# Performance work log

Measured on AMD Instinct MI355X. Metric: run time of the kernel, lower is better.

Reference implementation:

```python
import jax, jax.numpy as jnp
import numpy as np

TOKEN_ATTEND_SELF_VALUE = -0.0005
LN_EPS = 1e-5


def _layer_norm(x, g, b):
    mu = jnp.mean(x, axis=-1, keepdims=True)
    var = jnp.mean(jnp.square(x - mu), axis=-1, keepdims=True)
    return (x - mu) * jax.lax.rsqrt(var + LN_EPS) * g + b


def _gelu(x):
    return jax.nn.gelu(x, approximate=False)  # torch nn.GELU default is exact erf


def _grouped_ff(x, w1, b1, w2, b2):
    # x: [b, n, L, d]; per-level (grouped conv1d k=1) feedforward
    h = _gelu(jnp.einsum('bnld,ldm->bnlm', x, w1) + b1)
    return _gelu(jnp.einsum('bnlm,lmd->bnld', h, w2) + b2)


def _consensus_attention(levels):
    # levels: [b, n, L, d]; attend_self=False, no local mask
    b, n, L, d = levels.shape
    norm = jnp.maximum(jnp.linalg.norm(levels, axis=-1, keepdims=True), 1e-12)
    k = levels / norm  # F.normalize(dim=-1)
    sim = jnp.einsum('bild,bjld->blij', levels, k) * (d ** -0.5)
    eye = jnp.eye(n, dtype=bool)[None, None, :, :]
    sim = jnp.where(eye, TOKEN_ATTEND_SELF_VALUE, sim)
    attn = jax.nn.softmax(sim, axis=-1)
    return jnp.einsum('blij,bjld->bild', attn, levels)


def setup_inputs() -> dict:
    key = jax.random.key(0)
    ks = jax.random.split(key, 12)
    B, C, H, W = 2, 3, 48, 48
    dim, L = 32, 5
    n = H * W  # sub_patch_size = 1
    s = 0.02
    inp = {
        'img': jax.random.normal(ks[0], (B, C, H, W), jnp.float32),
        'w_tok': jax.random.normal(ks[1], (C, dim), jnp.float32) * s,
        'b_tok': jnp.zeros((dim,), jnp.float32),
        'g_ln_tok': jnp.ones((dim,), jnp.float32),
        'b_ln_tok': jnp.zeros((dim,), jnp.float32),
        'w_lvl': jax.random.normal(ks[2], (C, L * dim), jnp.float32) * s,
        'b_lvl': jnp.zeros((L * dim,), jnp.float32),
        'g_ln_lvl': jnp.ones((dim,), jnp.float32),
        'b_ln_lvl': jnp.zeros((dim,), jnp.float32),
        'pos_emb': jax.random.normal(ks[3], (n, dim), jnp.float32) * s,
        'bu_w1': jax.random.normal(ks[4], (L, dim, 4 * dim), jnp.float32) * s,
        'bu_b1': jnp.zeros((L, 4 * dim), jnp.float32),
        'bu_w2': jax.random.normal(ks[5], (L, 4 * dim, dim), jnp.float32) * s,
        'bu_b2': jnp.zeros((L, dim), jnp.float32),
        'td_w1': jax.random.normal(ks[6], (L - 1, dim, 4 * dim), jnp.float32) * s,
        'td_b1': jnp.zeros((L - 1, 4 * dim), jnp.float32),
        'td_w2': jax.random.normal(ks[7], (L - 1, 4 * dim, dim), jnp.float32) * s,
        'td_b2': jnp.zeros((L - 1, dim), jnp.float32),
        'iters': 3,
    }
    return inp


def reference(img, w_tok, b_tok, g_ln_tok, b_ln_tok, w_lvl, b_lvl, g_ln_lvl,
              b_ln_lvl, pos_emb, bu_w1, bu_b1, bu_w2, bu_b2, td_w1, td_b1,
              td_w2, td_b2, iters):
    B, C, H, W = img.shape
    L = bu_w1.shape[0]
    dim = w_tok.shape[1]
    x = jnp.transpose(img, (0, 2, 3, 1)).reshape(B, H * W, C)  # b n c

    # image_to_tokens: Linear -> LayerNorm -> GELU
    tokens = _gelu(_layer_norm(x @ w_tok + b_tok, g_ln_tok, b_ln_tok))  # [b,n,d]

    # image_to_levels: 1x1 Conv -> GELU -> reshape -> LayerNorm
    lv = _gelu(x @ w_lvl + b_lvl).reshape(B, H * W, L, dim)
    levels = _layer_norm(lv, g_ln_lvl, b_ln_lvl)  # [b,n,L,d]

    pos = pos_emb[None, :, None, :]  # () n () d
    bottom = tokens[:, :, None, :]  # [b,n,1,d]

    num_contrib = jnp.array([4.0] * (L - 1) + [3.0], jnp.float32)[None, None, :, None]

    for _ in range(iters):
        lwi = jnp.concatenate([bottom, levels], axis=2)  # [b,n,L+1,d]
        bu = _grouped_ff(lwi[:, :, :-1, :], bu_w1, bu_b1, bu_w2, bu_b2)
        td = _grouped_ff(lwi[:, :, 2:, :] + pos, td_w1, td_b1, td_w2, td_b2)
        td = jnp.pad(td, ((0, 0), (0, 0), (0, 1), (0, 0)))  # zero at top level
        cons = _consensus_attention(levels)
        levels = (levels + bu + td + cons) / num_contrib

    return levels
```

## Files before the change

### kernel.cpp

```cpp
#include <hip/hip_runtime.h>
#include <math.h>

#define BB 2
#define NN 2304
#define DIM 32
#define LL 5
#define HID 128
#define SJ 6
#define BLN (BB * LL * NN)
#define CONSGRID (SJ * 18 * LL * BB)
#define FFGRID (9 * 36)

#define QK_SCALE2 0.25503486f
#define SELF_VAL2 (-7.2134752e-4f)

typedef __attribute__((ext_vector_type(8))) short bf16x8;
typedef __attribute__((ext_vector_type(16))) float f32x16;

union B8U { bf16x8 v; unsigned u[4]; };

__device__ __forceinline__ unsigned bfb(float f) {
    union { float f; unsigned u; } c; c.f = f;
    return ((c.u + 0x7FFF + ((c.u >> 16) & 1)) >> 16) & 0xFFFFu;
}
__device__ __forceinline__ short bfs(float f) { return (short)bfb(f); }
__device__ __forceinline__ float b2f(unsigned bits16) {
    union { float f; unsigned u; } c; c.u = bits16 << 16; return c.f;
}
__device__ __forceinline__ unsigned cvt_pk_bf16(float lo, float hi) {
    unsigned r;
    asm("v_cvt_pk_bf16_f32 %0, %1, %2" : "=v"(r) : "v"(lo), "v"(hi));
    return r;
}

__device__ __forceinline__ float gelu_f(float v) {
    return 0.5f * v * (1.0f + erff(v * 0.70710678118654752f));
}

__device__ __forceinline__ void plswap(unsigned a, unsigned b, unsigned& o0, unsigned& o1) {
    auto r = __builtin_amdgcn_permlane32_swap(a, b, false, false);
    o0 = r[0]; o1 = r[1];
}

__global__ __launch_bounds__(256) void prep_all(
    const float* __restrict__ img,
    const float* __restrict__ w_tok, const float* __restrict__ b_tok,
    const float* __restrict__ g_ln_tok, const float* __restrict__ b_ln_tok,
    const float* __restrict__ w_lvl, const float* __restrict__ b_lvl,
    const float* __restrict__ g_ln_lvl, const float* __restrict__ b_ln_lvl,
    const float* __restrict__ pos_emb,
    const float* __restrict__ bu_w1, const float* __restrict__ bu_w2,
    const float* __restrict__ td_w1, const float* __restrict__ td_w2,
    float* __restrict__ levels, short* __restrict__ tokensB,
    short* __restrict__ Qb, short* __restrict__ Ksb, short* __restrict__ Vtb,
    short* __restrict__ TDb, short* __restrict__ W1T, short* __restrict__ W2T)
{
    int blk = blockIdx.x, tid = threadIdx.x;
    if (blk < 18) {
        int t = blk * 256 + tid;
        int b = t / NN, i = t - b * NN;
        float x0 = img[(size_t)(b * 3 + 0) * NN + i];
        float x1 = img[(size_t)(b * 3 + 1) * NN + i];
        float x2 = img[(size_t)(b * 3 + 2) * NN + i];
        float v[DIM];
        float mu = 0.f;
        #pragma unroll
        for (int m = 0; m < DIM; ++m) {
            v[m] = x0 * w_tok[m] + x1 * w_tok[DIM + m] + x2 * w_tok[2 * DIM + m] + b_tok[m];
            mu += v[m];
        }
        mu *= (1.0f / DIM);
        float var = 0.f;
        #pragma unroll
        for (int m = 0; m < DIM; ++m) { float dd = v[m] - mu; var += dd * dd; }
        var *= (1.0f / DIM);
        float rs = rsqrtf(var + 1e-5f);
        unsigned tw[16];
        #pragma unroll
        for (int d2 = 0; d2 < 16; ++d2) {
            float ya = gelu_f((v[2 * d2] - mu) * rs * g_ln_tok[2 * d2] + b_ln_tok[2 * d2]);
            float yb = gelu_f((v[2 * d2 + 1] - mu) * rs * g_ln_tok[2 * d2 + 1] + b_ln_tok[2 * d2 + 1]);
            tw[d2] = cvt_pk_bf16(ya, yb);
        }
        uint4* tp = (uint4*)(tokensB + (size_t)t * DIM);
        #pragma unroll
        for (int k4 = 0; k4 < 4; ++k4)
            tp[k4] = make_uint4(tw[4 * k4], tw[4 * k4 + 1], tw[4 * k4 + 2], tw[4 * k4 + 3]);
    } else if (blk < 108) {
        int z = blk - 18;
        int b = z / 45, rem = z % 45;
        int l = rem / 9, ic = rem % 9;
        int i = ic * 256 + tid;
        int t = b * NN + i;
        float x0 = img[(size_t)(b * 3 + 0) * NN + i];
        float x1 = img[(size_t)(b * 3 + 1) * NN + i];
        float x2 = img[(size_t)(b * 3 + 2) * NN + i];
        float u[DIM];
        float mu = 0.f;
        #pragma unroll
        for (int m = 0; m < DIM; ++m) {
            int c = l * DIM + m;
            float pre = x0 * w_lvl[c] + x1 * w_lvl[LL * DIM + c] + x2 * w_lvl[2 * LL * DIM + c] + b_lvl[c];
            u[m] = gelu_f(pre);
            mu += u[m];
        }
        mu *= (1.0f / DIM);
        float var = 0.f;
        #pragma unroll
        for (int m = 0; m < DIM; ++m) { float dd = u[m] - mu; var += dd * dd; }
        var *= (1.0f / DIM);
        float rs = rsqrtf(var + 1e-5f);
        float y[DIM];
        float n2 = 0.f;
        #pragma unroll
        for (int m = 0; m < DIM; ++m) {
            y[m] = (u[m] - mu) * rs * g_ln_lvl[m] + b_ln_lvl[m];
            levels[((size_t)t * LL + l) * DIM + m] = y[m];
            n2 += y[m] * y[m];
        }
        float ksc = QK_SCALE2 / fmaxf(sqrtf(n2), 1e-12f);
        size_t qro = ((size_t)(b * LL + l) * NN + i) * DIM;
        unsigned qw[16], kw[16];
        #pragma unroll
        for (int d2 = 0; d2 < 16; ++d2) {
            qw[d2] = cvt_pk_bf16(y[2 * d2], y[2 * d2 + 1]);
            kw[d2] = cvt_pk_bf16(y[2 * d2] * ksc, y[2 * d2 + 1] * ksc);
        }
        uint4* qp = (uint4*)(Qb + qro);
        uint4* kp = (uint4*)(Ksb + qro);
        #pragma unroll
        for (int k4 = 0; k4 < 4; ++k4) {
            qp[k4] = make_uint4(qw[4 * k4], qw[4 * k4 + 1], qw[4 * k4 + 2], qw[4 * k4 + 3]);
            kp[k4] = make_uint4(kw[4 * k4], kw[4 * k4 + 1], kw[4 * k4 + 2], kw[4 * k4 + 3]);
        }
        #pragma unroll
        for (int d = 0; d < DIM; ++d)
            Vtb[((size_t)(b * LL + l) * DIM + d) * NN + i] = bfs(y[d]);
        if (l >= 1) {
            unsigned dw[16];
            #pragma unroll
            for (int d2 = 0; d2 < 16; ++d2) {
                float p0 = pos_emb[(size_t)i * DIM + 2 * d2];
                float p1 = pos_emb[(size_t)i * DIM + 2 * d2 + 1];
                dw[d2] = cvt_pk_bf16(y[2 * d2] + p0, y[2 * d2 + 1] + p1);
            }
            uint4* dp = (uint4*)(TDb + ((size_t)(b * 4 + (l - 1)) * NN + i) * DIM);
            #pragma unroll
            for (int k4 = 0; k4 < 4; ++k4)
                dp[k4] = make_uint4(dw[4 * k4], dw[4 * k4 + 1], dw[4 * k4 + 2], dw[4 * k4 + 3]);
        }
    } else {
        int g = blk - 108;
        bool is_bu = g < LL;
        int lw = is_bu ? g : g - LL;
        const float* W1 = (is_bu ? bu_w1 : td_w1) + (size_t)lw * DIM * HID;
        const float* W2 = (is_bu ? bu_w2 : td_w2) + (size_t)lw * HID * DIM;
        short* o1 = W1T + (size_t)g * HID * DIM;
        short* o2 = W2T + (size_t)g * DIM * HID;
        for (int e = tid; e < HID * DIM; e += 256) {
            int m = e >> 5, d = e & 31;
            o1[e] = bfs(W1[(size_t)d * HID + m]);
            int dd = e >> 7, mm = e & 127;
            o2[e] = bfs(W2[(size_t)mm * DIM + dd]);
        }
    }
}

__global__ __launch_bounds__(256) void cons_ff(
    const short* __restrict__ Qb, const short* __restrict__ Ksb,
    const short* __restrict__ Vtb,
    const short* __restrict__ tokensB, const short* __restrict__ TDb,
    const short* __restrict__ W1T, const short* __restrict__ W2T,
    const float* __restrict__ bu_b1, const float* __restrict__ bu_b2,
    const float* __restrict__ td_b1, const float* __restrict__ td_b2,
    short* __restrict__ accp, float* __restrict__ sump,
    float* __restrict__ bu_out, float* __restrict__ td_out)
{
    __shared__ float b1_lds[HID];
    __shared__ float b2_lds[DIM];
    __shared__ __align__(16) float yt_lds[4][DIM * 32];

    int tid = threadIdx.x;
    int w = tid >> 6, lane = tid & 63;
    int li = lane & 31, hi = lane >> 5;

    if (blockIdx.x < CONSGRID) {
        int bid = blockIdx.x;
        int s = bid % SJ; int rest = bid / SJ;
        int ibig = rest % 18; rest /= 18;
        int l = rest % 5, b = rest / 5;
        int i0 = ibig * 128 + w * 32;

        const short* Qrow = Qb + (size_t)(b * LL + l) * NN * DIM;
        const short* Krow = Ksb + (size_t)(b * LL + l) * NN * DIM;
        const short* Vrow = Vtb + (size_t)(b * LL + l) * DIM * NN;

        bf16x8 qf0 = *(const bf16x8*)(Qrow + (size_t)(i0 + li) * DIM + hi * 8);
        bf16x8 qf1 = *(const bf16x8*)(Qrow + (size_t)(i0 + li) * DIM + 16 + hi * 8);

        f32x16 outacc = {};
        float ssum = 0.f;

        for (int jt = 0; jt < NN / SJ / 32; ++jt) {
            int j0 = s * (NN / SJ) + jt * 32;
            bf16x8 kf0 = *(const bf16x8*)(Krow + (size_t)(j0 + li) * DIM + hi * 8);
            bf16x8 kf1 = *(const bf16x8*)(Krow + (size_t)(j0 + li) * DIM + 16 + hi * 8);
            f32x16 st = {};
            st = __builtin_amdgcn_mfma_f32_32x32x16_bf16(kf0, qf0, st, 0, 0, 0);
            st = __builtin_amdgcn_mfma_f32_32x32x16_bf16(kf1, qf1, st, 0, 0, 0);
            float e[16];
            bool dg = (j0 == i0);
            #pragma unroll
            for (int r = 0; r < 16; ++r) {
                float sc = st[r];
                if (dg && (((r & 3) + 8 * (r >> 2) + 4 * hi) == li)) sc = SELF_VAL2;
                e[r] = exp2f(sc);
            }
            #pragma unroll
            for (int r = 0; r < 16; ++r) ssum += e[r];
            unsigned wpk[8];
            #pragma unroll
            for (int h2 = 0; h2 < 8; ++h2)
                wpk[h2] = cvt_pk_bf16(e[2 * h2], e[2 * h2 + 1]);
            B8U pa0, pa1;
            plswap(wpk[0], wpk[2], pa0.u[0], pa0.u[2]);
            plswap(wpk[1], wpk[3], pa0.u[1], pa0.u[3]);
            plswap(wpk[4], wpk[6], pa1.u[0], pa1.u[2]);
            plswap(wpk[5], wpk[7], pa1.u[1], pa1.u[3]);
            bf16x8 vf0 = *(const bf16x8*)(Vrow + (size_t)li * NN + j0 + hi * 8);
            bf16x8 vf1 = *(const bf16x8*)(Vrow + (size_t)li * NN + j0 + 16 + hi * 8);
            outacc = __builtin_amdgcn_mfma_f32_32x32x16_bf16(pa0.v, vf0, outacc, 0, 0, 0);
            outacc = __builtin_amdgcn_mfma_f32_32x32x16_bf16(pa1.v, vf1, outacc, 0, 0, 0);
        }
        size_t base = (size_t)s * BLN + (size_t)(b * LL + l) * NN;
        float ss2 = ssum + __shfl_xor(ssum, 32, 64);
        if (lane < 32) sump[base + i0 + li] = ss2;
        #pragma unroll
        for (int r = 0; r < 16; ++r) {
            int il = (r & 3) + 8 * (r >> 2) + 4 * hi;
            accp[(base + i0 + il) * DIM + li] = bfs(outacc[r]);
        }
    } else {
        int fb = blockIdx.x - CONSGRID;
        int g = fb / 36;
        int tile = fb % 36;

        bool is_bu = g < LL;
        int lw = is_bu ? g : g - LL;
        const float* B1 = (is_bu ? bu_b1 : td_b1) + (size_t)lw * HID;
        const float* B2 = (is_bu ? bu_b2 : td_b2) + (size_t)lw * DIM;
        if (tid < HID) b1_lds[tid] = B1[tid];
        if (tid < DIM) b2_lds[tid] = B2[tid];
        __syncthreads();

        int t0 = tile * 128 + w * 32;
        int b = t0 / NN;
        int i0 = t0 - b * NN;
        const short* xrow =
            (g == 0) ? (tokensB + (size_t)t0 * DIM)
          : is_bu    ? (Qb + ((size_t)(b * LL + (g - 1)) * NN + i0) * DIM)
                     : (TDb + ((size_t)(b * 4 + (g - LL)) * NN + i0) * DIM);
        const short* w1g = W1T + (size_t)g * HID * DIM;
        const short* w2g = W2T + (size_t)g * DIM * HID;

        bf16x8 xb0 = *(const bf16x8*)(xrow + (size_t)li * DIM + hi * 8);
        bf16x8 xb1 = *(const bf16x8*)(xrow + (size_t)li * DIM + 16 + hi * 8);

        f32x16 yacc = {};
        #pragma unroll
        for (int ht = 0; ht < 4; ++ht) {
            bf16x8 a0 = *(const bf16x8*)(w1g + (size_t)(ht * 32 + li) * DIM + hi * 8);
            bf16x8 a1 = *(const bf16x8*)(w1g + (size_t)(ht * 32 + li) * DIM + 16 + hi * 8);
            f32x16 hT = {};
            hT = __builtin_amdgcn_mfma_f32_32x32x16_bf16(a0, xb0, hT, 0, 0, 0);
            hT = __builtin_amdgcn_mfma_f32_32x32x16_bf16(a1, xb1, hT, 0, 0, 0);
            float h[16];
            #pragma unroll
            for (int r = 0; r < 16; ++r) {
                int lrow = (r & 3) + 8 * (r >> 2) + 4 * hi;
                h[r] = gelu_f(hT[r] + b1_lds[ht * 32 + lrow]);
            }
            unsigned wp[8];
            #pragma unroll
            for (int h2 = 0; h2 < 8; ++h2)
                wp[h2] = cvt_pk_bf16(h[2 * h2], h[2 * h2 + 1]);
            B8U hb0, hb1;
            plswap(wp[0], wp[2], hb0.u[0], hb0.u[2]);
            plswap(wp[1], wp[3], hb0.u[1], hb0.u[3]);
            plswap(wp[4], wp[6], hb1.u[0], hb1.u[2]);
            plswap(wp[5], wp[7], hb1.u[1], hb1.u[3]);
            bf16x8 a2 = *(const bf16x8*)(w2g + (size_t)li * HID + ht * 32 + hi * 8);
            bf16x8 a3 = *(const bf16x8*)(w2g + (size_t)li * HID + ht * 32 + 16 + hi * 8);
            yacc = __builtin_amdgcn_mfma_f32_32x32x16_bf16(a2, hb0.v, yacc, 0, 0, 0);
            yacc = __builtin_amdgcn_mfma_f32_32x32x16_bf16(a3, hb1.v, yacc, 0, 0, 0);
        }
        float* yt = yt_lds[w];
        #pragma unroll
        for (int r = 0; r < 16; ++r) {
            int dr = (r & 3) + 8 * (r >> 2) + 4 * hi;
            yt[dr * 32 + li] = gelu_f(yacc[r] + b2_lds[dr]);
        }
        int tk = lane >> 1, dh = (lane & 1) * 16;
        float ov[16];
        #pragma unroll
        for (int j = 0; j < 16; ++j) ov[j] = yt[(dh + j) * 32 + tk];
        float* op = (is_bu ? bu_out : td_out) + ((size_t)(t0 + tk) * LL + lw) * DIM + dh;
        #pragma unroll
        for (int j4 = 0; j4 < 4; ++j4)
            ((float4*)op)[j4] = make_float4(ov[4 * j4], ov[4 * j4 + 1], ov[4 * j4 + 2], ov[4 * j4 + 3]);
    }
}

__global__ __launch_bounds__(256) void combine8(
    const float* __restrict__ levels, const float* __restrict__ bu_buf,
    const float* __restrict__ td_buf, const float* __restrict__ pos_emb,
    const short* __restrict__ accp, const float* __restrict__ sump,
    float* __restrict__ levels_next,
    short* __restrict__ Qb, short* __restrict__ Ksb, short* __restrict__ Vtb,
    short* __restrict__ TDb)
{
    int rw = blockIdx.x * 32 + (threadIdx.x >> 3);
    int dq = threadIdx.x & 7;
    int d0 = dq * 4;
    int b = rw / (LL * NN);
    int l = (rw / NN) % LL;
    int i = rw % NN;
    size_t ro = (size_t)rw;

    float ssum = 0.f;
    #pragma unroll
    for (int s = 0; s < SJ; ++s) ssum += sump[(size_t)s * BLN + ro];
    float inv_s = 1.0f / ssum;
    float nc = (l == LL - 1) ? (1.0f / 3.0f) : 0.25f;

    float ax[4] = {0.f, 0.f, 0.f, 0.f};
    #pragma unroll
    for (int s = 0; s < SJ; ++s) {
        uint2 av = *(const uint2*)(accp + ((size_t)s * BLN + ro) * DIM + d0);
        ax[0] += b2f(av.x & 0xFFFFu);
        ax[1] += b2f(av.x >> 16);
        ax[2] += b2f(av.y & 0xFFFFu);
        ax[3] += b2f(av.y >> 16);
    }

    size_t lo = ((size_t)(b * NN + i) * LL + l) * DIM + d0;
    float4 lv = *(const float4*)(levels + lo);
    float4 bu = *(const float4*)(bu_buf + lo);
    float4 td = (l < LL - 1) ? *(const float4*)(td_buf + lo) : make_float4(0.f, 0.f, 0.f, 0.f);

    float o[4];
    o[0] = (lv.x + bu.x + td.x + ax[0] * inv_s) * nc;
    o[1] = (lv.y + bu.y + td.y + ax[1] * inv_s) * nc;
    o[2] = (lv.z + bu.z + td.z + ax[2] * inv_s) * nc;
    o[3] = (lv.w + bu.w + td.w + ax[3] * inv_s) * nc;
    *(float4*)(levels_next + lo) = make_float4(o[0], o[1], o[2], o[3]);

    float n2p = o[0] * o[0] + o[1] * o[1] + o[2] * o[2] + o[3] * o[3];
    n2p += __shfl_xor(n2p, 1, 64);
    n2p += __shfl_xor(n2p, 2, 64);
    n2p += __shfl_xor(n2p, 4, 64);
    float ksc = QK_SCALE2 / fmaxf(sqrtf(n2p), 1e-12f);

    size_t qro = ro * DIM + d0;
    unsigned q0 = cvt_pk_bf16(o[0], o[1]);
    unsigned q1 = cvt_pk_bf16(o[2], o[3]);
    unsigned k0 = cvt_pk_bf16(o[0] * ksc, o[1] * ksc);
    unsigned k1 = cvt_pk_bf16(o[2] * ksc, o[3] * ksc);
    *(uint2*)(Qb + qro)  = make_uint2(q0, q1);
    *(uint2*)(Ksb + qro) = make_uint2(k0, k1);
    #pragma unroll
    for (int d = 0; d < 4; ++d)
        Vtb[((size_t)(b * LL + l) * DIM + d0 + d) * NN + i] = bfs(o[d]);
    if (l >= 1) {
        float p0 = pos_emb[(size_t)i * DIM + d0 + 0];
        float p1 = pos_emb[(size_t)i * DIM + d0 + 1];
        float p2 = pos_emb[(size_t)i * DIM + d0 + 2];
        float p3 = pos_emb[(size_t)i * DIM + d0 + 3];
        unsigned t0 = cvt_pk_bf16(o[0] + p0, o[1] + p1);
        unsigned t1 = cvt_pk_bf16(o[2] + p2, o[3] + p3);
        *(uint2*)(TDb + ((size_t)(b * 4 + (l - 1)) * NN + i) * DIM + d0) = make_uint2(t0, t1);
    }
}

extern "C" void kernel_launch(void* const* d_in, const int* in_sizes, int n_in,
                              void* d_out, int out_size, void* d_ws, size_t ws_size,
                              hipStream_t stream)
{
    (void)in_sizes; (void)n_in; (void)out_size; (void)ws_size;
    const float* img      = (const float*)d_in[0];
    const float* w_tok    = (const float*)d_in[1];
    const float* b_tok    = (const float*)d_in[2];
    const float* g_ln_tok = (const float*)d_in[3];
    const float* b_ln_tok = (const float*)d_in[4];
    const float* w_lvl    = (const float*)d_in[5];
    const float* b_lvl    = (const float*)d_in[6];
    const float* g_ln_lvl = (const float*)d_in[7];
    const float* b_ln_lvl = (const float*)d_in[8];
    const float* pos_emb  = (const float*)d_in[9];
    const float* bu_w1    = (const float*)d_in[10];
    const float* bu_b1    = (const float*)d_in[11];
    const float* bu_w2    = (const float*)d_in[12];
    const float* bu_b2    = (const float*)d_in[13];
    const float* td_w1    = (const float*)d_in[14];
    const float* td_b1    = (const float*)d_in[15];
    const float* td_w2    = (const float*)d_in[16];
    const float* td_b2    = (const float*)d_in[17];

    float* ws      = (float*)d_ws;
    float* levelsA = ws;
    float* levelsB = levelsA + (size_t)BB * NN * LL * DIM;
    float* bu_buf  = levelsB + (size_t)BB * NN * LL * DIM;
    float* td_buf  = bu_buf  + (size_t)BB * NN * LL * DIM;
    float* sump    = td_buf  + (size_t)BB * NN * LL * DIM;
    short* accp    = (short*)(sump + (size_t)SJ * BLN);
    short* Qb      = accp + (size_t)SJ * BLN * DIM;
    short* Ksb     = Qb   + (size_t)BLN * DIM;
    short* Vtb     = Ksb  + (size_t)BLN * DIM;
    short* tokensB = Vtb  + (size_t)BLN * DIM;
    short* TDb     = tokensB + (size_t)BB * NN * DIM;
    short* W1T     = TDb  + (size_t)BB * 4 * NN * DIM;
    short* W2T     = W1T  + (size_t)9 * HID * DIM;
    float* outp    = (float*)d_out;

    const int cfGrid   = CONSGRID + FFGRID;
    const int combGrid = BLN / 32;

    prep_all<<<117, 256, 0, stream>>>(
        img, w_tok, b_tok, g_ln_tok, b_ln_tok, w_lvl, b_lvl, g_ln_lvl, b_ln_lvl,
        pos_emb, bu_w1, bu_w2, td_w1, td_w2,
        levelsA, tokensB, Qb, Ksb, Vtb, TDb, W1T, W2T);

    cons_ff<<<cfGrid, 256, 0, stream>>>(Qb, Ksb, Vtb, tokensB, TDb, W1T, W2T,
        bu_b1, bu_b2, td_b1, td_b2, accp, sump, bu_buf, td_buf);
    combine8<<<combGrid, 256, 0, stream>>>(levelsA, bu_buf, td_buf, pos_emb,
        accp, sump, levelsB, Qb, Ksb, Vtb, TDb);

    cons_ff<<<cfGrid, 256, 0, stream>>>(Qb, Ksb, Vtb, tokensB, TDb, W1T, W2T,
        bu_b1, bu_b2, td_b1, td_b2, accp, sump, bu_buf, td_buf);
    combine8<<<combGrid, 256, 0, stream>>>(levelsB, bu_buf, td_buf, pos_emb,
        accp, sump, levelsA, Qb, Ksb, Vtb, TDb);

    cons_ff<<<cfGrid, 256, 0, stream>>>(Qb, Ksb, Vtb, tokensB, TDb, W1T, W2T,
        bu_b1, bu_b2, td_b1, td_b2, accp, sump, bu_buf, td_buf);
    combine8<<<combGrid, 256, 0, stream>>>(levelsA, bu_buf, td_buf, pos_emb,
        accp, sump, outp, Qb, Ksb, Vtb, TDb);
}
```

Baseline: 137.6 us.

## Fuse all stages into one cooperative persistent kernel with grid syncs

Replaces the seven separate launches (prep, then three rounds of attention/FF and combine) with a single cooperative kernel of 512 blocks. The blocks loop over the virtual block indices of each stage and separate the stages with grid.sync(). This is meant to remove kernel launch gaps and tail idle time between stages. In exchange, each stage now runs on a fixed grid with grid-stride loops, and occupancy is capped by the two-blocks-per-CU launch bound. If the cooperative launch fails, the code falls back to the old multi-launch sequence.

Result: slower. 535.2 us (+289.0%).

```diff
diff --git a/kernel.cpp b/kernel.cpp
--- a/kernel.cpp
+++ b/kernel.cpp
@@ -1,5 +1,8 @@
 #include <hip/hip_runtime.h>
+#include <hip/hip_cooperative_groups.h>
 #include <math.h>
+
+namespace cg = cooperative_groups;
 
 #define BB 2
 #define NN 2304
@@ -10,6 +13,8 @@
 #define BLN (BB * LL * NN)
 #define CONSGRID (SJ * 18 * LL * BB)
 #define FFGRID (9 * 36)
+#define COMBGRID (BLN / 32)
+#define COOPGRID 512
 
 #define QK_SCALE2 0.25503486f
 #define SELF_VAL2 (-7.2134752e-4f)
@@ -32,41 +37,36 @@
     asm("v_cvt_pk_bf16_f32 %0, %1, %2" : "=v"(r) : "v"(lo), "v"(hi));
     return r;
 }
-
 __device__ __forceinline__ float gelu_f(float v) {
     return 0.5f * v * (1.0f + erff(v * 0.70710678118654752f));
 }
-
 __device__ __forceinline__ void plswap(unsigned a, unsigned b, unsigned& o0, unsigned& o1) {
     auto r = __builtin_amdgcn_permlane32_swap(a, b, false, false);
     o0 = r[0]; o1 = r[1];
 }
 
-__global__ __launch_bounds__(256) void prep_all(
-    const float* __restrict__ img,
-    const float* __restrict__ w_tok, const float* __restrict__ b_tok,
-    const float* __restrict__ g_ln_tok, const float* __restrict__ b_ln_tok,
-    const float* __restrict__ w_lvl, const float* __restrict__ b_lvl,
-    const float* __restrict__ g_ln_lvl, const float* __restrict__ b_ln_lvl,
-    const float* __restrict__ pos_emb,
-    const float* __restrict__ bu_w1, const float* __restrict__ bu_w2,
-    const float* __restrict__ td_w1, const float* __restrict__ td_w2,
-    float* __restrict__ levels, short* __restrict__ tokensB,
-    short* __restrict__ Qb, short* __restrict__ Ksb, short* __restrict__ Vtb,
-    short* __restrict__ TDb, short* __restrict__ W1T, short* __restrict__ W2T)
-{
-    int blk = blockIdx.x, tid = threadIdx.x;
+struct MegaP {
+    const float *img, *w_tok, *b_tok, *g_ln_tok, *b_ln_tok;
+    const float *w_lvl, *b_lvl, *g_ln_lvl, *b_ln_lvl, *pos_emb;
+    const float *bu_w1, *bu_b1, *bu_w2, *bu_b2;
+    const float *td_w1, *td_b1, *td_w2, *td_b2;
+    float *levelsA, *levelsB, *bu_buf, *td_buf, *sump;
+    short *accp, *Qb, *Ksb, *Vtb, *tokensB, *TDb, *W1T, *W2T;
+    float *outp;
+};
+
+__device__ __forceinline__ void prep_body(int blk, int tid, const MegaP& p) {
     if (blk < 18) {
         int t = blk * 256 + tid;
         int b = t / NN, i = t - b * NN;
-        float x0 = img[(size_t)(b * 3 + 0) * NN + i];
-        float x1 = img[(size_t)(b * 3 + 1) * NN + i];
-        float x2 = img[(size_t)(b * 3 + 2) * NN + i];
+        float x0 = p.img[(size_t)(b * 3 + 0) * NN + i];
+        float x1 = p.img[(size_t)(b * 3 + 1) * NN + i];
+        float x2 = p.img[(size_t)(b * 3 + 2) * NN + i];
         float v[DIM];
         float mu = 0.f;
         #pragma unroll
         for (int m = 0; m < DIM; ++m) {
-            v[m] = x0 * w_tok[m] + x1 * w_tok[DIM + m] + x2 * w_tok[2 * DIM + m] + b_tok[m];
+            v[m] = x0 * p.w_tok[m] + x1 * p.w_tok[DIM + m] + x2 * p.w_tok[2 * DIM + m] + p.b_tok[m];
             mu += v[m];
         }
         mu *= (1.0f / DIM);
@@ -78,11 +78,11 @@
         unsigned tw[16];
         #pragma unroll
         for (int d2 = 0; d2 < 16; ++d2) {
-            float ya = gelu_f((v[2 * d2] - mu) * rs * g_ln_tok[2 * d2] + b_ln_tok[2 * d2]);
-            float yb = gelu_f((v[2 * d2 + 1] - mu) * rs * g_ln_tok[2 * d2 + 1] + b_ln_tok[2 * d2 + 1]);
+            float ya = gelu_f((v[2 * d2] - mu) * rs * p.g_ln_tok[2 * d2] + p.b_ln_tok[2 * d2]);
+            float yb = gelu_f((v[2 * d2 + 1] - mu) * rs * p.g_ln_tok[2 * d2 + 1] + p.b_ln_tok[2 * d2 + 1]);
             tw[d2] = cvt_pk_bf16(ya, yb);
         }
-        uint4* tp = (uint4*)(tokensB + (size_t)t * DIM);
+        uint4* tp = (uint4*)(p.tokensB + (size_t)t * DIM);
         #pragma unroll
         for (int k4 = 0; k4 < 4; ++k4)
             tp[k4] = make_uint4(tw[4 * k4], tw[4 * k4 + 1], tw[4 * k4 + 2], tw[4 * k4 + 3]);
@@ -92,15 +92,15 @@
         int l = rem / 9, ic = rem % 9;
         int i = ic * 256 + tid;
         int t = b * NN + i;
-        float x0 = img[(size_t)(b * 3 + 0) * NN + i];
-        float x1 = img[(size_t)(b * 3 + 1) * NN + i];
-        float x2 = img[(size_t)(b * 3 + 2) * NN + i];
+        float x0 = p.img[(size_t)(b * 3 + 0) * NN + i];
+        float x1 = p.img[(size_t)(b * 3 + 1) * NN + i];
+        float x2 = p.img[(size_t)(b * 3 + 2) * NN + i];
         float u[DIM];
         float mu = 0.f;
         #pragma unroll
         for (int m = 0; m < DIM; ++m) {
             int c = l * DIM + m;
-            float pre = x0 * w_lvl[c] + x1 * w_lvl[LL * DIM + c] + x2 * w_lvl[2 * LL * DIM + c] + b_lvl[c];
+            float pre = x0 * p.w_lvl[c] + x1 * p.w_lvl[LL * DIM + c] + x2 * p.w_lvl[2 * LL * DIM + c] + p.b_lvl[c];
             u[m] = gelu_f(pre);
             mu += u[m];
         }
@@ -114,8 +114,8 @@
         float n2 = 0.f;
         #pragma unroll
         for (int m = 0; m < DIM; ++m) {
-            y[m] = (u[m] - mu) * rs * g_ln_lvl[m] + b_ln_lvl[m];
-            levels[((size_t)t * LL + l) * DIM + m] = y[m];
+            y[m] = (u[m] - mu) * rs * p.g_ln_lvl[m] + p.b_ln_lvl[m];
+            p.levelsA[((size_t)t * LL + l) * DIM + m] = y[m];
             n2 += y[m] * y[m];
         }
         float ksc = QK_SCALE2 / fmaxf(sqrtf(n2), 1e-12f);
@@ -126,8 +126,8 @@
             qw[d2] = cvt_pk_bf16(y[2 * d2], y[2 * d2 + 1]);
             kw[d2] = cvt_pk_bf16(y[2 * d2] * ksc, y[2 * d2 + 1] * ksc);
         }
-        uint4* qp = (uint4*)(Qb + qro);
-        uint4* kp = (uint4*)(Ksb + qro);
+        uint4* qp = (uint4*)(p.Qb + qro);
+        uint4* kp = (uint4*)(p.Ksb + qro);
         #pragma unroll
         for (int k4 = 0; k4 < 4; ++k4) {
             qp[k4] = make_uint4(qw[4 * k4], qw[4 * k4 + 1], qw[4 * k4 + 2], qw[4 * k4 + 3]);
@@ -135,16 +135,16 @@
         }
         #pragma unroll
         for (int d = 0; d < DIM; ++d)
-            Vtb[((size_t)(b * LL + l) * DIM + d) * NN + i] = bfs(y[d]);
+            p.Vtb[((size_t)(b * LL + l) * DIM + d) * NN + i] = bfs(y[d]);
         if (l >= 1) {
             unsigned dw[16];
             #pragma unroll
             for (int d2 = 0; d2 < 16; ++d2) {
-                float p0 = pos_emb[(size_t)i * DIM + 2 * d2];
-                float p1 = pos_emb[(size_t)i * DIM + 2 * d2 + 1];
+                float p0 = p.pos_emb[(size_t)i * DIM + 2 * d2];
+                float p1 = p.pos_emb[(size_t)i * DIM + 2 * d2 + 1];
                 dw[d2] = cvt_pk_bf16(y[2 * d2] + p0, y[2 * d2 + 1] + p1);
             }
-            uint4* dp = (uint4*)(TDb + ((size_t)(b * 4 + (l - 1)) * NN + i) * DIM);
+            uint4* dp = (uint4*)(p.TDb + ((size_t)(b * 4 + (l - 1)) * NN + i) * DIM);
             #pragma unroll
             for (int k4 = 0; k4 < 4; ++k4)
                 dp[k4] = make_uint4(dw[4 * k4], dw[4 * k4 + 1], dw[4 * k4 + 2], dw[4 * k4 + 3]);
@@ -153,10 +153,10 @@
         int g = blk - 108;
         bool is_bu = g < LL;
         int lw = is_bu ? g : g - LL;
-        const float* W1 = (is_bu ? bu_w1 : td_w1) + (size_t)lw * DIM * HID;
-        const float* W2 = (is_bu ? bu_w2 : td_w2) + (size_t)lw * HID * DIM;
-        short* o1 = W1T + (size_t)g * HID * DIM;
-        short* o2 = W2T + (size_t)g * DIM * HID;
+        const float* W1 = (is_bu ? p.bu_w1 : p.td_w1) + (size_t)lw * DIM * HID;
+        const float* W2 = (is_bu ? p.bu_w2 : p.td_w2) + (size_t)lw * HID * DIM;
+        short* o1 = p.W1T + (size_t)g * HID * DIM;
+        short* o2 = p.W2T + (size_t)g * DIM * HID;
         for (int e = tid; e < HID * DIM; e += 256) {
             int m = e >> 5, d = e & 31;
             o1[e] = bfs(W1[(size_t)d * HID + m]);
@@ -166,161 +166,142 @@
     }
 }
 
-__global__ __launch_bounds__(256) void cons_ff(
-    const short* __restrict__ Qb, const short* __restrict__ Ksb,
-    const short* __restrict__ Vtb,
-    const short* __restrict__ tokensB, const short* __restrict__ TDb,
-    const short* __restrict__ W1T, const short* __restrict__ W2T,
-    const float* __restrict__ bu_b1, const float* __restrict__ bu_b2,
-    const float* __restrict__ td_b1, const float* __restrict__ td_b2,
-    short* __restrict__ accp, float* __restrict__ sump,
-    float* __restrict__ bu_out, float* __restrict__ td_out)
-{
-    __shared__ float b1_lds[HID];
-    __shared__ float b2_lds[DIM];
-    __shared__ __align__(16) float yt_lds[4][DIM * 32];
-
-    int tid = threadIdx.x;
+__device__ __forceinline__ void cons_body(int bid, int tid, const MegaP& p) {
     int w = tid >> 6, lane = tid & 63;
     int li = lane & 31, hi = lane >> 5;
-
-    if (blockIdx.x < CONSGRID) {
-        int bid = blockIdx.x;
-        int s = bid % SJ; int rest = bid / SJ;
-        int ibig = rest % 18; rest /= 18;
-        int l = rest % 5, b = rest / 5;
-        int i0 = ibig * 128 + w * 32;
-
-        const short* Qrow = Qb + (size_t)(b * LL + l) * NN * DIM;
-        const short* Krow = Ksb + (size_t)(b * LL + l) * NN * DIM;
-        const short* Vrow = Vtb + (size_t)(b * LL + l) * DIM * NN;
-
-        bf16x8 qf0 = *(const bf16x8*)(Qrow + (size_t)(i0 + li) * DIM + hi * 8);
-        bf16x8 qf1 = *(const bf16x8*)(Qrow + (size_t)(i0 + li) * DIM + 16 + hi * 8);
-
-        f32x16 outacc = {};
-        float ssum = 0.f;
-
-        for (int jt = 0; jt < NN / SJ / 32; ++jt) {
-            int j0 = s * (NN / SJ) + jt * 32;
-            bf16x8 kf0 = *(const bf16x8*)(Krow + (size_t)(j0 + li) * DIM + hi * 8);
-            bf16x8 kf1 = *(const bf16x8*)(Krow + (size_t)(j0 + li) * DIM + 16 + hi * 8);
-            f32x16 st = {};
-            st = __builtin_amdgcn_mfma_f32_32x32x16_bf16(kf0, qf0, st, 0, 0, 0);
-            st = __builtin_amdgcn_mfma_f32_32x32x16_bf16(kf1, qf1, st, 0, 0, 0);
-            float e[16];
-            bool dg = (j0 == i0);
-            #pragma unroll
-            for (int r = 0; r < 16; ++r) {
-                float sc = st[r];
-                if (dg && (((r & 3) + 8 * (r >> 2) + 4 * hi) == li)) sc = SELF_VAL2;
-                e[r] = exp2f(sc);
-            }
-            #pragma unroll
-            for (int r = 0; r < 16; ++r) ssum += e[r];
-            unsigned wpk[8];
-            #pragma unroll
-            for (int h2 = 0; h2 < 8; ++h2)
-                wpk[h2] = cvt_pk_bf16(e[2 * h2], e[2 * h2 + 1]);
-            B8U pa0, pa1;
-            plswap(wpk[0], wpk[2], pa0.u[0], pa0.u[2]);
-            plswap(wpk[1], wpk[3], pa0.u[1], pa0.u[3]);
-            plswap(wpk[4], wpk[6], pa1.u[0], pa1.u[2]);
-            plswap(wpk[5], wpk[7], pa1.u[1], pa1.u[3]);
-            bf16x8 vf0 = *(const bf16x8*)(Vrow + (size_t)li * NN + j0 + hi * 8);
-            bf16x8 vf1 = *(const bf16x8*)(Vrow + (size_t)li * NN + j0 + 16 + hi * 8);
-            outacc = __builtin_amdgcn_mfma_f32_32x32x16_bf16(pa0.v, vf0, outacc, 0, 0, 0);
-            outacc = __builtin_amdgcn_mfma_f32_32x32x16_bf16(pa1.v, vf1, outacc, 0, 0, 0);
-        }
-        size_t base = (size_t)s * BLN + (size_t)(b * LL + l) * NN;
-        float ss2 = ssum + __shfl_xor(ssum, 32, 64);
-        if (lane < 32) sump[base + i0 + li] = ss2;
+    int s = bid % SJ; int rest = bid / SJ;
+    int ibig = rest % 18; rest /= 18;
+    int l = rest % 5, b = rest / 5;
+    int i0 = ibig * 128 + w * 32;
+
+    const short* Qrow = p.Qb + (size_t)(b * LL + l) * NN * DIM;
+    const short* Krow = p.Ksb + (size_t)(b * LL + l) * NN * DIM;
+    const short* Vrow = p.Vtb + (size_t)(b * LL + l) * DIM * NN;
+
+    bf16x8 qf0 = *(const bf16x8*)(Qrow + (size_t)(i0 + li) * DIM + hi * 8);
+    bf16x8 qf1 = *(const bf16x8*)(Qrow + (size_t)(i0 + li) * DIM + 16 + hi * 8);
+
+    f32x16 outacc = {};
+    float ssum = 0.f;
+
+    for (int jt = 0; jt < NN / SJ / 32; ++jt) {
+        int j0 = s * (NN / SJ) + jt * 32;
+        bf16x8 kf0 = *(const bf16x8*)(Krow + (size_t)(j0 + li) * DIM + hi * 8);
+        bf16x8 kf1 = *(const bf16x8*)(Krow + (size_t)(j0 + li) * DIM + 16 + hi * 8);
+        f32x16 st = {};
+        st = __builtin_amdgcn_mfma_f32_32x32x16_bf16(kf0, qf0, st, 0, 0, 0);
+        st = __builtin_amdgcn_mfma_f32_32x32x16_bf16(kf1, qf1, st, 0, 0, 0);
+        float e[16];
+        bool dg = (j0 == i0);
         #pragma unroll
         for (int r = 0; r < 16; ++r) {
-            int il = (r & 3) + 8 * (r >> 2) + 4 * hi;
-            accp[(base + i0 + il) * DIM + li] = bfs(outacc[r]);
-        }
-    } else {
-        int fb = blockIdx.x - CONSGRID;
-        int g = fb / 36;
-        int tile = fb % 36;
-
-        bool is_bu = g < LL;
-        int lw = is_bu ? g : g - LL;
-        const float* B1 = (is_bu ? bu_b1 : td_b1) + (size_t)lw * HID;
-        const float* B2 = (is_bu ? bu_b2 : td_b2) + (size_t)lw * DIM;
-        if (tid < HID) b1_lds[tid] = B1[tid];
-        if (tid < DIM) b2_lds[tid] = B2[tid];
-        __syncthreads();
-
-        int t0 = tile * 128 + w * 32;
-        int b = t0 / NN;
-        int i0 = t0 - b * NN;
-        const short* xrow =
-            (g == 0) ? (tokensB + (size_t)t0 * DIM)
-          : is_bu    ? (Qb + ((size_t)(b * LL + (g - 1)) * NN + i0) * DIM)
-                     : (TDb + ((size_t)(b * 4 + (g - LL)) * NN + i0) * DIM);
-        const short* w1g = W1T + (size_t)g * HID * DIM;
-        const short* w2g = W2T + (size_t)g * DIM * HID;
-
-        bf16x8 xb0 = *(const bf16x8*)(xrow + (size_t)li * DIM + hi * 8);
-        bf16x8 xb1 = *(const bf16x8*)(xrow + (size_t)li * DIM + 16 + hi * 8);
-
-        f32x16 yacc = {};
-        #pragma unroll
-        for (int ht = 0; ht < 4; ++ht) {
-            bf16x8 a0 = *(const bf16x8*)(w1g + (size_t)(ht * 32 + li) * DIM + hi * 8);
-            bf16x8 a1 = *(const bf16x8*)(w1g + (size_t)(ht * 32 + li) * DIM + 16 + hi * 8);
-            f32x16 hT = {};
-            hT = __builtin_amdgcn_mfma_f32_32x32x16_bf16(a0, xb0, hT, 0, 0, 0);
-            hT = __builtin_amdgcn_mfma_f32_32x32x16_bf16(a1, xb1, hT, 0, 0, 0);
-            float h[16];
-            #pragma unroll
-            for (int r = 0; r < 16; ++r) {
-                int lrow = (r & 3) + 8 * (r >> 2) + 4 * hi;
-                h[r] = gelu_f(hT[r] + b1_lds[ht * 32 + lrow]);
-            }
-            unsigned wp[8];
-            #pragma unroll
-            for (int h2 = 0; h2 < 8; ++h2)
-                wp[h2] = cvt_pk_bf16(h[2 * h2], h[2 * h2 + 1]);
-            B8U hb0, hb1;
-            plswap(wp[0], wp[2], hb0.u[0], hb0.u[2]);
-            plswap(wp[1], wp[3], hb0.u[1], hb0.u[3]);
-            plswap(wp[4], wp[6], hb1.u[0], hb1.u[2]);
-            plswap(wp[5], wp[7], hb1.u[1], hb1.u[3]);
-            bf16x8 a2 = *(const bf16x8*)(w2g + (size_t)li * HID + ht * 32 + hi * 8);
-            bf16x8 a3 = *(const bf16x8*)(w2g + (size_t)li * HID + ht * 32 + 16 + hi * 8);
-            yacc = __builtin_amdgcn_mfma_f32_32x32x16_bf16(a2, hb0.v, yacc, 0, 0, 0);
-            yacc = __builtin_amdgcn_mfma_f32_32x32x16_bf16(a3, hb1.v, yacc, 0, 0, 0);
-        }
-        float* yt = yt_lds[w];
+            float sc = st[r];
+            if (dg && (((r & 3) + 8 * (r >> 2) + 4 * hi) == li)) sc = SELF_VAL2;
+            e[r] = exp2f(sc);
+        }
+        #pragma unroll
+        for (int r = 0; r < 16; ++r) ssum += e[r];
+        unsigned wpk[8];
+        #pragma unroll
+        for (int h2 = 0; h2 < 8; ++h2)
+            wpk[h2] = cvt_pk_bf16(e[2 * h2], e[2 * h2 + 1]);
+        B8U pa0, pa1;
+        plswap(wpk[0], wpk[2], pa0.u[0], pa0.u[2]);
+        plswap(wpk[1], wpk[3], pa0.u[1], pa0.u[3]);
+        plswap(wpk[4], wpk[6], pa1.u[0], pa1.u[2]);
+        plswap(wpk[5], wpk[7], pa1.u[1], pa1.u[3]);
+        bf16x8 vf0 = *(const bf16x8*)(Vrow + (size_t)li * NN + j0 + hi * 8);
+        bf16x8 vf1 = *(const bf16x8*)(Vrow + (size_t)li * NN + j0 + 16 + hi * 8);
+        outacc = __builtin_amdgcn_mfma_f32_32x32x16_bf16(pa0.v, vf0, outacc, 0, 0, 0);
+        outacc = __builtin_amdgcn_mfma_f32_32x32x16_bf16(pa1.v, vf1, outacc, 0, 0, 0);
+    }
+    size_t base = (size_t)s * BLN + (size_t)(b * LL + l) * NN;
+    float ss2 = ssum + __shfl_xor(ssum, 32, 64);
+    if (lane < 32) p.sump[base + i0 + li] = ss2;
+    #pragma unroll
+    for (int r = 0; r < 16; ++r) {
+        int il = (r & 3) + 8 * (r >> 2) + 4 * hi;
+        p.accp[(base + i0 + il) * DIM + li] = bfs(outacc[r]);
+    }
+}
+
+__device__ __forceinline__ void ff_body(int fb, int tid, const MegaP& p,
+                                        float* b1_lds, float* b2_lds, float* yt_base) {
+    int w = tid >> 6, lane = tid & 63;
+    int li = lane & 31, hi = lane >> 5;
+    int g = fb / 36;
+    int tile = fb % 36;
+
+    bool is_bu = g < LL;
+    int lw = is_bu ? g : g - LL;
+    const float* B1 = (is_bu ? p.bu_b1 : p.td_b1) + (size_t)lw * HID;
+    const float* B2 = (is_bu ? p.bu_b2 : p.td_b2) + (size_t)lw * DIM;
+    __syncthreads();
+    if (tid < HID) b1_lds[tid] = B1[tid];
+    if (tid < DIM) b2_lds[tid] = B2[tid];
+    __syncthreads();
+
+    int t0 = tile * 128 + w * 32;
+    int b = t0 / NN;
+    int i0 = t0 - b * NN;
+    const short* xrow =
+        (g == 0) ? (p.tokensB + (size_t)t0 * DIM)
+      : is_bu    ? (p.Qb + ((size_t)(b * LL + (g - 1)) * NN + i0) * DIM)
+                 : (p.TDb + ((size_t)(b * 4 + (g - LL)) * NN + i0) * DIM);
+    const short* w1g = p.W1T + (size_t)g * HID * DIM;
+    const short* w2g = p.W2T + (size_t)g * DIM * HID;
+
+    bf16x8 xb0 = *(const bf16x8*)(xrow + (size_t)li * DIM + hi * 8);
+    bf16x8 xb1 = *(const bf16x8*)(xrow + (size_t)li * DIM + 16 + hi * 8);
+
+    f32x16 yacc = {};
+    #pragma unroll
+    for (int ht = 0; ht < 4; ++ht) {
+        bf16x8 a0 = *(const bf16x8*)(w1g + (size_t)(ht * 32 + li) * DIM + hi * 8);
+        bf16x8 a1 = *(const bf16x8*)(w1g + (size_t)(ht * 32 + li) * DIM + 16 + hi * 8);
+        f32x16 hT = {};
+        hT = __builtin_amdgcn_mfma_f32_32x32x16_bf16(a0, xb0, hT, 0, 0, 0);
+        hT = __builtin_amdgcn_mfma_f32_32x32x16_bf16(a1, xb1, hT, 0, 0, 0);
+        float h[16];
         #pragma unroll
         for (int r = 0; r < 16; ++r) {
-            int dr = (r & 3) + 8 * (r >> 2) + 4 * hi;
-            yt[dr * 32 + li] = gelu_f(yacc[r] + b2_lds[dr]);
-        }
-        int tk = lane >> 1, dh = (lane & 1) * 16;
-        float ov[16];
-        #pragma unroll
-        for (int j = 0; j < 16; ++j) ov[j] = yt[(dh + j) * 32 + tk];
-        float* op = (is_bu ? bu_out : td_out) + ((size_t)(t0 + tk) * LL + lw) * DIM + dh;
-        #pragma unroll
-        for (int j4 = 0; j4 < 4; ++j4)
-            ((float4*)op)[j4] = make_float4(ov[4 * j4], ov[4 * j4 + 1], ov[4 * j4 + 2], ov[4 * j4 + 3]);
-    }
-}
-
-__global__ __launch_bounds__(256) void combine8(
-    const float* __restrict__ levels, const float* __restrict__ bu_buf,
-    const float* __restrict__ td_buf, const float* __restrict__ pos_emb,
-    const short* __restrict__ accp, const float* __restrict__ sump,
-    float* __restrict__ levels_next,
-    short* __restrict__ Qb, short* __restrict__ Ksb, short* __restrict__ Vtb,
-    short* __restrict__ TDb)
-{
-    int rw = blockIdx.x * 32 + (threadIdx.x >> 3);
-    int dq = threadIdx.x & 7;
+            int lrow = (r & 3) + 8 * (r >> 2) + 4 * hi;
+            h[r] = gelu_f(hT[r] + b1_lds[ht * 32 + lrow]);
+        }
+        unsigned wp[8];
+        #pragma unroll
+        for (int h2 = 0; h2 < 8; ++h2)
+            wp[h2] = cvt_pk_bf16(h[2 * h2], h[2 * h2 + 1]);
+        B8U hb0, hb1;
+        plswap(wp[0], wp[2], hb0.u[0], hb0.u[2]);
+        plswap(wp[1], wp[3], hb0.u[1], hb0.u[3]);
+        plswap(wp[4], wp[6], hb1.u[0], hb1.u[2]);
+        plswap(wp[5], wp[7], hb1.u[1], hb1.u[3]);
+        bf16x8 a2 = *(const bf16x8*)(w2g + (size_t)li * HID + ht * 32 + hi * 8);
+        bf16x8 a3 = *(const bf16x8*)(w2g + (size_t)li * HID + ht * 32 + 16 + hi * 8);
+        yacc = __builtin_amdgcn_mfma_f32_32x32x16_bf16(a2, hb0.v, yacc, 0, 0, 0);
+        yacc = __builtin_amdgcn_mfma_f32_32x32x16_bf16(a3, hb1.v, yacc, 0, 0, 0);
+    }
+    float* yt = yt_base + w * (DIM * 32);
+    #pragma unroll
+    for (int r = 0; r < 16; ++r) {
+        int dr = (r & 3) + 8 * (r >> 2) + 4 * hi;
+        yt[dr * 32 + li] = gelu_f(yacc[r] + b2_lds[dr]);
+    }
+    int tk = lane >> 1, dh = (lane & 1) * 16;
+    float ov[16];
+    #pragma unroll
+    for (int j = 0; j < 16; ++j) ov[j] = yt[(dh + j) * 32 + tk];
+    float* op = (is_bu ? p.bu_buf : p.td_buf) + ((size_t)(t0 + tk) * LL + lw) * DIM + dh;
+    #pragma unroll
+    for (int j4 = 0; j4 < 4; ++j4)
+        ((float4*)op)[j4] = make_float4(ov[4 * j4], ov[4 * j4 + 1], ov[4 * j4 + 2], ov[4 * j4 + 3]);
+}
+
+__device__ __forceinline__ void combine_body(int blk, int tid, const MegaP& p,
+                                             const float* lv_in, float* lv_out) {
+    int rw = blk * 32 + (tid >> 3);
+    int dq = tid & 7;
     int d0 = dq * 4;
     int b = rw / (LL * NN);
     int l = (rw / NN) % LL;
@@ -329,14 +310,14 @@
 
     float ssum = 0.f;
     #pragma unroll
-    for (int s = 0; s < SJ; ++s) ssum += sump[(size_t)s * BLN + ro];
+    for (int s = 0; s < SJ; ++s) ssum += p.sump[(size_t)s * BLN + ro];
     float inv_s = 1.0f / ssum;
     float nc = (l == LL - 1) ? (1.0f / 3.0f) : 0.25f;
 
     float ax[4] = {0.f, 0.f, 0.f, 0.f};
     #pragma unroll
     for (int s = 0; s < SJ; ++s) {
-        uint2 av = *(const uint2*)(accp + ((size_t)s * BLN + ro) * DIM + d0);
+        uint2 av = *(const uint2*)(p.accp + ((size_t)s * BLN + ro) * DIM + d0);
         ax[0] += b2f(av.x & 0xFFFFu);
         ax[1] += b2f(av.x >> 16);
         ax[2] += b2f(av.y & 0xFFFFu);
@@ -344,16 +325,16 @@
     }
 
     size_t lo = ((size_t)(b * NN + i) * LL + l) * DIM + d0;
-    float4 lv = *(const float4*)(levels + lo);
-    float4 bu = *(const float4*)(bu_buf + lo);
-    float4 td = (l < LL - 1) ? *(const float4*)(td_buf + lo) : make_float4(0.f, 0.f, 0.f, 0.f);
+    float4 lv = *(const float4*)(lv_in + lo);
+    float4 bu = *(const float4*)(p.bu_buf + lo);
+    float4 td = (l < LL - 1) ? *(const float4*)(p.td_buf + lo) : make_float4(0.f, 0.f, 0.f, 0.f);
 
     float o[4];
     o[0] = (lv.x + bu.x + td.x + ax[0] * inv_s) * nc;
     o[1] = (lv.y + bu.y + td.y + ax[1] * inv_s) * nc;
     o[2] = (lv.z + bu.z + td.z + ax[2] * inv_s) * nc;
     o[3] = (lv.w + bu.w + td.w + ax[3] * inv_s) * nc;
-    *(float4*)(levels_next + lo) = make_float4(o[0], o[1], o[2], o[3]);
+    *(float4*)(lv_out + lo) = make_float4(o[0], o[1], o[2], o[3]);
 
     float n2p = o[0] * o[0] + o[1] * o[1] + o[2] * o[2] + o[3] * o[3];
     n2p += __shfl_xor(n2p, 1, 64);
@@ -366,20 +347,60 @@
     unsigned q1 = cvt_pk_bf16(o[2], o[3]);
     unsigned k0 = cvt_pk_bf16(o[0] * ksc, o[1] * ksc);
     unsigned k1 = cvt_pk_bf16(o[2] * ksc, o[3] * ksc);
-    *(uint2*)(Qb + qro)  = make_uint2(q0, q1);
-    *(uint2*)(Ksb + qro) = make_uint2(k0, k1);
+    *(uint2*)(p.Qb + qro)  = make_uint2(q0, q1);
+    *(uint2*)(p.Ksb + qro) = make_uint2(k0, k1);
     #pragma unroll
     for (int d = 0; d < 4; ++d)
-        Vtb[((size_t)(b * LL + l) * DIM + d0 + d) * NN + i] = bfs(o[d]);
+        p.Vtb[((size_t)(b * LL + l) * DIM + d0 + d) * NN + i] = bfs(o[d]);
     if (l >= 1) {
-        float p0 = pos_emb[(size_t)i * DIM + d0 + 0];
-        float p1 = pos_emb[(size_t)i * DIM + d0 + 1];
-        float p2 = pos_emb[(size_t)i * DIM + d0 + 2];
-        float p3 = pos_emb[(size_t)i * DIM + d0 + 3];
+        float p0 = p.pos_emb[(size_t)i * DIM + d0 + 0];
+        float p1 = p.pos_emb[(size_t)i * DIM + d0 + 1];
+        float p2 = p.pos_emb[(size_t)i * DIM + d0 + 2];
+        float p3 = p.pos_emb[(size_t)i * DIM + d0 + 3];
         unsigned t0 = cvt_pk_bf16(o[0] + p0, o[1] + p1);
         unsigned t1 = cvt_pk_bf16(o[2] + p2, o[3] + p3);
-        *(uint2*)(TDb + ((size_t)(b * 4 + (l - 1)) * NN + i) * DIM + d0) = make_uint2(t0, t1);
-    }
+        *(uint2*)(p.TDb + ((size_t)(b * 4 + (l - 1)) * NN + i) * DIM + d0) = make_uint2(t0, t1);
+    }
+}
+
+__global__ __launch_bounds__(256, 2) void mega(MegaP p) {
+    __shared__ float b1_lds[HID];
+    __shared__ float b2_lds[DIM];
+    __shared__ __align__(16) float yt_lds[4][DIM * 32];
+    cg::grid_group grid = cg::this_grid();
+    int tid = threadIdx.x;
+
+    for (int vb = blockIdx.x; vb < 117; vb += gridDim.x)
+        prep_body(vb, tid, p);
+    grid.sync();
+
+    #pragma unroll 1
+    for (int it = 0; it < 3; ++it) {
+        const float* lv_in = (it == 1) ? p.levelsB : p.levelsA;
+        float* lv_out      = (it == 0) ? p.levelsB : (it == 1) ? p.levelsA : p.outp;
+        for (int vb = blockIdx.x; vb < CONSGRID + FFGRID; vb += gridDim.x) {
+            if (vb < CONSGRID) cons_body(vb, tid, p);
+            else ff_body(vb - CONSGRID, tid, p, b1_lds, b2_lds, &yt_lds[0][0]);
+        }
+        grid.sync();
+        for (int vb = blockIdx.x; vb < COMBGRID; vb += gridDim.x)
+            combine_body(vb, tid, p, lv_in, lv_out);
+        if (it < 2) grid.sync();
+    }
+}
+
+__global__ __launch_bounds__(256) void prep_k(MegaP p) {
+    prep_body(blockIdx.x, threadIdx.x, p);
+}
+__global__ __launch_bounds__(256) void consff_k(MegaP p) {
+    __shared__ float b1_lds[HID];
+    __shared__ float b2_lds[DIM];
+    __shared__ __align__(16) float yt_lds[4][DIM * 32];
+    if (blockIdx.x < CONSGRID) cons_body(blockIdx.x, threadIdx.x, p);
+    else ff_body(blockIdx.x - CONSGRID, threadIdx.x, p, b1_lds, b2_lds, &yt_lds[0][0]);
+}
+__global__ __launch_bounds__(256) void combine_k(MegaP p, const float* lv_in, float* lv_out) {
+    combine_body(blockIdx.x, threadIdx.x, p, lv_in, lv_out);
 }
 
 extern "C" void kernel_launch(void* const* d_in, const int* in_sizes, int n_in,
@@ -387,25 +408,6 @@
                               hipStream_t stream)
 {
     (void)in_sizes; (void)n_in; (void)out_size; (void)ws_size;
-    const float* img      = (const float*)d_in[0];
-    const float* w_tok    = (const float*)d_in[1];
-    const float* b_tok    = (const float*)d_in[2];
-    const float* g_ln_tok = (const float*)d_in[3];
-    const float* b_ln_tok = (const float*)d_in[4];
-    const float* w_lvl    = (const float*)d_in[5];
-    const float* b_lvl    = (const float*)d_in[6];
-    const float* g_ln_lvl = (const float*)d_in[7];
-    const float* b_ln_lvl = (const float*)d_in[8];
-    const float* pos_emb  = (const float*)d_in[9];
-    const float* bu_w1    = (const float*)d_in[10];
-    const float* bu_b1    = (const float*)d_in[11];
-    const float* bu_w2    = (const float*)d_in[12];
-    const float* bu_b2    = (const float*)d_in[13];
-    const float* td_w1    = (const float*)d_in[14];
-    const float* td_b1    = (const float*)d_in[15];
-    const float* td_w2    = (const float*)d_in[16];
-    const float* td_b2    = (const float*)d_in[17];
-
     float* ws      = (float*)d_ws;
     float* levelsA = ws;
     float* levelsB = levelsA + (size_t)BB * NN * LL * DIM;
@@ -420,28 +422,42 @@
     short* TDb     = tokensB + (size_t)BB * NN * DIM;
     short* W1T     = TDb  + (size_t)BB * 4 * NN * DIM;
     short* W2T     = W1T  + (size_t)9 * HID * DIM;
-    float* outp    = (float*)d_out;
-
-    const int cfGrid   = CONSGRID + FFGRID;
-    const int combGrid = BLN / 32;
-
-    prep_all<<<117, 256, 0, stream>>>(
-        img, w_tok, b_tok, g_ln_tok, b_ln_tok, w_lvl, b_lvl, g_ln_lvl, b_ln_lvl,
-        pos_emb, bu_w1, bu_w2, td_w1, td_w2,
-        levelsA, tokensB, Qb, Ksb, Vtb, TDb, W1T, W2T);
-
-    cons_ff<<<cfGrid, 256, 0, stream>>>(Qb, Ksb, Vtb, tokensB, TDb, W1T, W2T,
-        bu_b1, bu_b2, td_b1, td_b2, accp, sump, bu_buf, td_buf);
-    combine8<<<combGrid, 256, 0, stream>>>(levelsA, bu_buf, td_buf, pos_emb,
-        accp, sump, levelsB, Qb, Ksb, Vtb, TDb);
-
-    cons_ff<<<cfGrid, 256, 0, stream>>>(Qb, Ksb, Vtb, tokensB, TDb, W1T, W2T,
-        bu_b1, bu_b2, td_b1, td_b2, accp, sump, bu_buf, td_buf);
-    combine8<<<combGrid, 256, 0, stream>>>(levelsB, bu_buf, td_buf, pos_emb,
-        accp, sump, levelsA, Qb, Ksb, Vtb, TDb);
-
-    cons_ff<<<cfGrid, 256, 0, stream>>>(Qb, Ksb, Vtb, tokensB, TDb, W1T, W2T,
-        bu_b1, bu_b2, td_b1, td_b2, accp, sump, bu_buf, td_buf);
-    combine8<<<combGrid, 256, 0, stream>>>(levelsA, bu_buf, td_buf, pos_emb,
-        accp, sump, outp, Qb, Ksb, Vtb, TDb);
-}
+
+    MegaP hp;
+    hp.img      = (const float*)d_in[0];
+    hp.w_tok    = (const float*)d_in[1];
+    hp.b_tok    = (const float*)d_in[2];
+    hp.g_ln_tok = (const float*)d_in[3];
+    hp.b_ln_tok = (const float*)d_in[4];
+    hp.w_lvl    = (const float*)d_in[5];
+    hp.b_lvl    = (const float*)d_in[6];
+    hp.g_ln_lvl = (const float*)d_in[7];
+    hp.b_ln_lvl = (const float*)d_in[8];
+    hp.pos_emb  = (const float*)d_in[9];
+    hp.bu_w1    = (const float*)d_in[10];
+    hp.bu_b1    = (const float*)d_in[11];
+    hp.bu_w2    = (const float*)d_in[12];
+    hp.bu_b2    = (const float*)d_in[13];
+    hp.td_w1    = (const float*)d_in[14];
+    hp.td_b1    = (const float*)d_in[15];
+    hp.td_w2    = (const float*)d_in[16];
+    hp.td_b2    = (const float*)d_in[17];
+    hp.levelsA = levelsA; hp.levelsB = levelsB;
+    hp.bu_buf = bu_buf; hp.td_buf = td_buf; hp.sump = sump;
+    hp.accp = accp; hp.Qb = Qb; hp.Ksb = Ksb; hp.Vtb = Vtb;
+    hp.tokensB = tokensB; hp.TDb = TDb; hp.W1T = W1T; hp.W2T = W2T;
+    hp.outp = (float*)d_out;
+
+    void* args[] = { &hp };
+    hipError_t e = hipLaunchCooperativeKernel((void*)mega, dim3(COOPGRID), dim3(256),
+                                              args, 0, stream);
+    if (e != hipSuccess) {
+        prep_k<<<117, 256, 0, stream>>>(hp);
+        consff_k<<<CONSGRID + FFGRID, 256, 0, stream>>>(hp);
+        combine_k<<<COMBGRID, 256, 0, stream>>>(hp, levelsA, levelsB);
+        consff_k<<<CONSGRID + FFGRID, 256, 0, stream>>>(hp);
+        combine_k<<<COMBGRID, 256, 0, stream>>>(hp, levelsB, levelsA);
+        consff_k<<<CONSGRID + FFGRID, 256, 0, stream>>>(hp);
+        combine_k<<<COMBGRID, 256, 0, stream>>>(hp, levelsA, (float*)d_out);
+    }
+}
```
